# Optimization experiments

Measured on AMD Instinct MI355X. Metric: run time of the kernel, lower is better.

The kernel has to match this reference:

```python
import jax, jax.numpy as jnp
import numpy as np

B, N, D, H, T = 2048, 128, 256, 8, 64
HD = D // H
TANH_C = 10.0
MASK_PENALTY = 1e9


def setup_inputs() -> dict:
    key = jax.random.key(0)
    ks = jax.random.split(key, 16)
    s = 1.0 / np.sqrt(D).astype(np.float32)
    w = lambda k: jax.random.normal(k, (D, D), jnp.float32) * s
    return {
        'node_emb': jax.random.normal(ks[0], (B, N, D), jnp.float32),
        'graph_emb': jax.random.normal(ks[1], (B, D), jnp.float32),
        'W_target': w(ks[2]), 'W_global': w(ks[3]),
        'W_K1': w(ks[4]), 'W_K2': w(ks[5]),
        'W_Q': w(ks[6]), 'W_V': w(ks[7]),
        'Wq_m': w(ks[8]), 'Wk_m': w(ks[9]), 'Wv_m': w(ks[10]), 'Wo_m': w(ks[11]),
        'targets': jax.random.randint(ks[12], (T, B), 0, N, jnp.int32),
        'masks': jax.random.randint(ks[13], (T, B, N), 0, 2, jnp.int32),
    }


def _mha(q, k, v, Wq, Wk, Wv, Wo):
    # q: [B,1,D]; k,v: [B,N,D]. Standard multi-head attention (glimpse).
    qh = (q @ Wq.T).reshape(B, 1, H, HD).transpose(0, 2, 1, 3)   # [B,H,1,HD]
    kh = (k @ Wk.T).reshape(B, N, H, HD).transpose(0, 2, 1, 3)   # [B,H,N,HD]
    vh = (v @ Wv.T).reshape(B, N, H, HD).transpose(0, 2, 1, 3)
    scores = jnp.einsum('bhqd,bhnd->bhqn', qh, kh) / np.sqrt(HD).astype(np.float32)
    attn = jax.nn.softmax(scores, axis=-1)
    out = jnp.einsum('bhqn,bhnd->bhqd', attn, vh)                # [B,H,1,HD]
    out = out.transpose(0, 2, 1, 3).reshape(B, 1, D)
    return out @ Wo.T


def reference(node_emb, graph_emb, W_target, W_global, W_K1, W_K2, W_Q, W_V,
              Wq_m, Wk_m, Wv_m, Wo_m, targets, masks):
    # Step-invariant projections (embeddings fixed across decode steps here).
    keys = node_emb @ W_K1.T      # [B,N,D]
    vals = node_emb @ W_V.T       # [B,N,D]
    key2 = node_emb @ W_K2.T      # [B,N,D]
    g_ctx = graph_emb @ W_global.T  # [B,D]
    inv_sqrt_d = np.float32(1.0 / np.sqrt(D))

    def step(ll, tm):
        tgt, mask = tm  # tgt:[B] int32, mask:[B,N] int32
        tgt_emb = jnp.take_along_axis(node_emb, tgt[:, None, None], axis=1)[:, 0, :]  # [B,D]
        context = (tgt_emb @ W_target.T + g_ctx)[:, None, :]      # [B,1,D]
        glimpse = _mha(context, keys, vals, Wq_m, Wk_m, Wv_m, Wo_m)  # [B,1,D]
        query = glimpse @ W_Q.T                                    # [B,1,D]
        logits = jnp.einsum('bqd,bnd->bn', query, key2) * inv_sqrt_d  # [B,N]
        logits = TANH_C * jnp.tanh(logits) - mask.astype(jnp.float32) * MASK_PENALTY
        log_p = jax.nn.log_softmax(logits, axis=1)
        actions = jnp.argmax(log_p, axis=1)                        # greedy TopKSampler
        ll = ll + jnp.take_along_axis(log_p, actions[:, None], axis=1)[:, 0]
        return ll, None

    ll, _ = jax.lax.scan(step, jnp.zeros(B, jnp.float32), (targets, masks))
    return ll
```

## Files before the change

kernel.cpp:

```cpp
#include <hip/hip_runtime.h>
#include <hip/hip_bf16.h>

#define BB 2048
#define NN 128
#define DD 256
#define HH 8
#define TT 64

typedef __bf16 bf16x8 __attribute__((ext_vector_type(8)));
typedef float f32x4 __attribute__((ext_vector_type(4)));

static __device__ __forceinline__ f32x4 mfma16(bf16x8 a, bf16x8 b, f32x4 c) {
  return __builtin_amdgcn_mfma_f32_16x16x32_bf16(a, b, c, 0, 0, 0);
}

static __device__ __forceinline__ f32x4 zero4() {
  f32x4 z = {0.f, 0.f, 0.f, 0.f};
  return z;
}

static __device__ __forceinline__ bf16x8 cvt8(const float* p) {
  const float4 x0 = *(const float4*)p;
  const float4 x1 = *(const float4*)(p + 4);
  bf16x8 r;
  r[0] = (__bf16)x0.x; r[1] = (__bf16)x0.y; r[2] = (__bf16)x0.z; r[3] = (__bf16)x0.w;
  r[4] = (__bf16)x1.x; r[5] = (__bf16)x1.y; r[6] = (__bf16)x1.z; r[7] = (__bf16)x1.w;
  return r;
}

static __device__ __forceinline__ unsigned pk2(float a, float b) {
  __bf16 x = (__bf16)a, y = (__bf16)b;
  unsigned short ux, uy;
  __builtin_memcpy(&ux, &x, 2);
  __builtin_memcpy(&uy, &y, 2);
  return (unsigned)ux | ((unsigned)uy << 16);
}

static __device__ __forceinline__ float fast_tanh10(float y) {
  const float e = __expf(2.f * y);
  return 10.f - 20.f * __builtin_amdgcn_rcpf(1.f + e);
}

__global__ void fold1(const float* __restrict__ Wq_m, const float* __restrict__ W_target,
                      const float* __restrict__ W_global, const float* __restrict__ Wk_m,
                      const float* __restrict__ W_K1, const float* __restrict__ Wv_m,
                      const float* __restrict__ W_V, const float* __restrict__ W_Q,
                      const float* __restrict__ Wo_m,
                      __bf16* __restrict__ WTQ, float* __restrict__ WGQT,
                      __bf16* __restrict__ WKH, __bf16* __restrict__ WVH,
                      float* __restrict__ WQO) {
  const int p = blockIdx.x >> 8;
  const int i = blockIdx.x & 255;
  const int t = threadIdx.x;
  __shared__ float arow[256];
  const float* A;
  const float* Bm;
  if (p == 0)      { A = Wq_m; Bm = W_target; }
  else if (p == 1) { A = Wq_m; Bm = W_global; }
  else if (p == 2) { A = Wk_m; Bm = W_K1; }
  else if (p == 3) { A = Wv_m; Bm = W_V; }
  else             { A = W_Q;  Bm = Wo_m; }
  arow[t] = A[i * 256 + t];
  __syncthreads();
  float acc = 0.f;
  for (int k = 0; k < 256; ++k) acc = fmaf(arow[k], Bm[k * 256 + t], acc);
  if (p == 0)      WTQ[i * 256 + t] = (__bf16)acc;
  else if (p == 1) WGQT[t * 256 + i] = acc;
  else if (p == 2) WKH[i * 256 + t] = (__bf16)acc;
  else if (p == 3) WVH[i * 256 + t] = (__bf16)acc;
  else             WQO[i * 256 + t] = acc;
}

__global__ void fold2(const float* __restrict__ WQO, const float* __restrict__ W_K2,
                      __bf16* __restrict__ WZL) {
  const int j = blockIdx.x;
  const int t = threadIdx.x;
  __shared__ float col[256];
  col[t] = W_K2[t * 256 + j];
  __syncthreads();
  float acc = 0.f;
  for (int d = 0; d < 256; ++d) acc = fmaf(WQO[d * 256 + t], col[d], acc);
  WZL[j * 256 + t] = (__bf16)acc;
}

__global__ void gq_kernel(const float* __restrict__ ge, const float* __restrict__ WGQT,
                          float* __restrict__ GQ) {
  const int b0 = blockIdx.x * 8;
  const int t = threadIdx.x;
  __shared__ float g[8][256];
#pragma unroll
  for (int i = 0; i < 8; ++i) g[i][t] = ge[(b0 + i) * 256 + t];
  __syncthreads();
  float acc[8] = {0.f, 0.f, 0.f, 0.f, 0.f, 0.f, 0.f, 0.f};
  for (int j = 0; j < 256; ++j) {
    const float wv = WGQT[j * 256 + t];
#pragma unroll
    for (int i = 0; i < 8; ++i) acc[i] = fmaf(wv, g[i][j], acc[i]);
  }
#pragma unroll
  for (int i = 0; i < 8; ++i) GQ[(b0 + i) * 256 + t] = acc[i];
}

__global__ __launch_bounds__(256)
void kv_kernel(const float* __restrict__ E, const __bf16* __restrict__ WKH,
               const __bf16* __restrict__ WVH, __bf16* __restrict__ KH,
               __bf16* __restrict__ VT, __bf16* __restrict__ Ebf) {
  const int b = blockIdx.x;
  const int tid = threadIdx.x;
  const int w = tid >> 6;
  const int l = tid & 63;
  const int lr = l & 15;
  const int lg = l >> 4;
  __shared__ __align__(16) __bf16 Es[128 * 264];
  const float* Eb = E + (size_t)b * NN * DD;
  __bf16* Ebfb = Ebf + (size_t)b * NN * DD;
  for (int c = tid; c < 4096; c += 256) {
    const int row = c >> 5;
    const int c8 = c & 31;
    const bf16x8 v = cvt8(Eb + row * 256 + c8 * 8);
    *(bf16x8*)&Es[row * 264 + c8 * 8] = v;
    *(bf16x8*)(Ebfb + row * 256 + c8 * 8) = v;
  }
  __syncthreads();

  {
    f32x4 acc[8][4];
#pragma unroll
    for (int mf = 0; mf < 8; ++mf)
#pragma unroll
      for (int nf = 0; nf < 4; ++nf) acc[mf][nf] = zero4();
    for (int kk = 0; kk < 8; ++kk) {
      bf16x8 aF[8], bF[4];
#pragma unroll
      for (int mf = 0; mf < 8; ++mf)
        aF[mf] = *(const bf16x8*)&Es[(mf * 16 + lr) * 264 + kk * 32 + lg * 8];
#pragma unroll
      for (int nf = 0; nf < 4; ++nf)
        bF[nf] = *(const bf16x8*)(WKH + (size_t)(w * 64 + nf * 16 + lr) * DD + kk * 32 + lg * 8);
#pragma unroll
      for (int mf = 0; mf < 8; ++mf)
#pragma unroll
        for (int nf = 0; nf < 4; ++nf) acc[mf][nf] = mfma16(aF[mf], bF[nf], acc[mf][nf]);
    }
    __bf16* KHb = KH + (size_t)b * NN * DD;
#pragma unroll
    for (int mf = 0; mf < 8; ++mf)
#pragma unroll
      for (int nf = 0; nf < 4; ++nf)
#pragma unroll
        for (int r = 0; r < 4; ++r)
          KHb[(mf * 16 + lg * 4 + r) * DD + w * 64 + nf * 16 + lr] = (__bf16)acc[mf][nf][r];
  }

  {
    f32x4 acc[4][8];
#pragma unroll
    for (int mf = 0; mf < 4; ++mf)
#pragma unroll
      for (int nf = 0; nf < 8; ++nf) acc[mf][nf] = zero4();
    for (int kk = 0; kk < 8; ++kk) {
      bf16x8 aW[4], bE[8];
#pragma unroll
      for (int mf = 0; mf < 4; ++mf)
        aW[mf] = *(const bf16x8*)(WVH + (size_t)(w * 64 + mf * 16 + lr) * DD + kk * 32 + lg * 8);
#pragma unroll
      for (int nf = 0; nf < 8; ++nf)
        bE[nf] = *(const bf16x8*)&Es[(nf * 16 + lr) * 264 + kk * 32 + lg * 8];
#pragma unroll
      for (int mf = 0; mf < 4; ++mf)
#pragma unroll
        for (int nf = 0; nf < 8; ++nf) acc[mf][nf] = mfma16(aW[mf], bE[nf], acc[mf][nf]);
    }
    __bf16* VTb = VT + (size_t)b * DD * NN;
#pragma unroll
    for (int mf = 0; mf < 4; ++mf)
#pragma unroll
      for (int nf = 0; nf < 8; ++nf)
#pragma unroll
        for (int r = 0; r < 4; ++r)
          VTb[(w * 64 + mf * 16 + lg * 4 + r) * NN + nf * 16 + lr] = (__bf16)acc[mf][nf][r];
  }
}

__global__ __launch_bounds__(256)
void qproj_kernel(const __bf16* __restrict__ Ebf, const int* __restrict__ tg,
                  const __bf16* __restrict__ WTQ, const float* __restrict__ GQ,
                  __bf16* __restrict__ Qb) {
  const int b = blockIdx.x;
  const int tid = threadIdx.x;
  const int w = tid >> 6;
  const int l = tid & 63;
  const int lr = l & 15;
  const int lg = l >> 4;
  __shared__ __align__(16) __bf16 Qst[64 * 264];
  __shared__ int tgs[64];
  if (tid < 64) tgs[tid] = tg[tid * BB + b];
  __syncthreads();
  const __bf16* Eb = Ebf + (size_t)b * NN * DD;
#pragma unroll
  for (int it = 0; it < 8; ++it) {
    const int c = it * 256 + tid;
    const int row = c >> 5;
    const int c8 = c & 31;
    *(bf16x8*)&Qst[row * 264 + c8 * 8] =
        *(const bf16x8*)(Eb + (size_t)tgs[row] * DD + c8 * 8);
  }
  __syncthreads();

  f32x4 acc[4][4];
#pragma unroll
  for (int mf = 0; mf < 4; ++mf)
#pragma unroll
    for (int nf = 0; nf < 4; ++nf) acc[mf][nf] = zero4();
  for (int kk = 0; kk < 8; ++kk) {
    bf16x8 aF[4], bF[4];
#pragma unroll
    for (int mf = 0; mf < 4; ++mf)
      aF[mf] = *(const bf16x8*)&Qst[(mf * 16 + lr) * 264 + kk * 32 + lg * 8];
#pragma unroll
    for (int nf = 0; nf < 4; ++nf)
      bF[nf] = *(const bf16x8*)(WTQ + (size_t)(w * 64 + nf * 16 + lr) * DD + kk * 32 + lg * 8);
#pragma unroll
    for (int mf = 0; mf < 4; ++mf)
#pragma unroll
      for (int nf = 0; nf < 4; ++nf) acc[mf][nf] = mfma16(aF[mf], bF[nf], acc[mf][nf]);
  }
#pragma unroll
  for (int nf = 0; nf < 4; ++nf) {
    const int col = w * 64 + nf * 16 + lr;
    const float g = GQ[b * DD + col];
#pragma unroll
    for (int mf = 0; mf < 4; ++mf)
#pragma unroll
      for (int r = 0; r < 4; ++r)
        Qb[((size_t)b * TT + mf * 16 + lg * 4 + r) * DD + col] = (__bf16)(acc[mf][nf][r] + g);
  }
}

__global__ __launch_bounds__(256)
void attn4_kernel(const __bf16* __restrict__ Qb, const __bf16* __restrict__ KH,
                  const __bf16* __restrict__ VT, __bf16* __restrict__ HO) {
  const int b = blockIdx.x >> 2;
  const int c0 = (blockIdx.x & 3) * 64;
  const int tid = threadIdx.x;
  const int w = tid >> 6;
  const int l = tid & 63;
  const int lr = l & 15;
  const int lg = l >> 4;
  const int T0 = w * 16;

  __shared__ __align__(16) __bf16 KHs[128 * 72];
  __shared__ __align__(16) __bf16 VTs[64 * 136];
  __shared__ __align__(16) __bf16 Ps[4][16 * 136];

  const __bf16* KHb = KH + (size_t)b * NN * DD;
  const __bf16* VTb = VT + (size_t)b * DD * NN;

#pragma unroll
  for (int it = 0; it < 4; ++it) {
    const int c = it * 256 + tid;
    const int row = c >> 3;
    const int c8 = c & 7;
    *(bf16x8*)&KHs[row * 72 + c8 * 8] = *(const bf16x8*)(KHb + (size_t)row * DD + c0 + c8 * 8);
  }
#pragma unroll
  for (int it = 0; it < 4; ++it) {
    const int c = it * 256 + tid;
    const int row = c >> 4;
    const int c8 = c & 15;
    *(bf16x8*)&VTs[row * 136 + c8 * 8] =
        *(const bf16x8*)(VTb + (size_t)(c0 + row) * NN + c8 * 8);
  }
  __syncthreads();

  __bf16* myp = Ps[w];
  __bf16* HOb = HO + (size_t)b * TT * DD + c0;

#pragma unroll
  for (int h = 0; h < 2; ++h) {
    const bf16x8 aq =
        *(const bf16x8*)(Qb + ((size_t)b * TT + T0 + lr) * DD + c0 + h * 32 + lg * 8);
    f32x4 s[8];
#pragma unroll
    for (int nf = 0; nf < 8; ++nf)
      s[nf] = mfma16(*(const bf16x8*)&KHs[(nf * 16 + lr) * 72 + h * 32 + lg * 8], aq, zero4());

    float mx = -1e30f;
#pragma unroll
    for (int nf = 0; nf < 8; ++nf)
#pragma unroll
      for (int r = 0; r < 4; ++r) mx = fmaxf(mx, s[nf][r]);
    mx = fmaxf(mx, __shfl_xor(mx, 16));
    mx = fmaxf(mx, __shfl_xor(mx, 32));

    float sm = 0.f;
    uint2 evp[8];
#pragma unroll
    for (int nf = 0; nf < 8; ++nf) {
      const float e0 = __expf((s[nf][0] - mx) * 0.17677669529663687f);
      const float e1 = __expf((s[nf][1] - mx) * 0.17677669529663687f);
      const float e2 = __expf((s[nf][2] - mx) * 0.17677669529663687f);
      const float e3 = __expf((s[nf][3] - mx) * 0.17677669529663687f);
      sm += (e0 + e1) + (e2 + e3);
      evp[nf].x = pk2(e0, e1);
      evp[nf].y = pk2(e2, e3);
    }
    sm += __shfl_xor(sm, 16);
    sm += __shfl_xor(sm, 32);

#pragma unroll
    for (int nf = 0; nf < 8; ++nf)
      *(uint2*)&myp[lr * 136 + nf * 16 + lg * 4] = evp[nf];

    f32x4 o0 = zero4(), o1 = zero4();
#pragma unroll
    for (int kk = 0; kk < 4; ++kk) {
      const bf16x8 ap = *(const bf16x8*)&myp[lr * 136 + kk * 32 + lg * 8];
      o0 = mfma16(ap, *(const bf16x8*)&VTs[(h * 32 + lr) * 136 + kk * 32 + lg * 8], o0);
      o1 = mfma16(ap, *(const bf16x8*)&VTs[(h * 32 + 16 + lr) * 136 + kk * 32 + lg * 8], o1);
    }
#pragma unroll
    for (int r = 0; r < 4; ++r) {
      const float inv = __builtin_amdgcn_rcpf(__shfl(sm, lg * 4 + r));
      HOb[(size_t)(T0 + lg * 4 + r) * DD + h * 32 + lr] = (__bf16)(o0[r] * inv);
      HOb[(size_t)(T0 + lg * 4 + r) * DD + h * 32 + 16 + lr] = (__bf16)(o1[r] * inv);
    }
  }
}

__global__ __launch_bounds__(256)
void zlog2_kernel(const __bf16* __restrict__ Ebf, const __bf16* __restrict__ HO,
                  const __bf16* __restrict__ WZL, const int* __restrict__ MK,
                  float* __restrict__ out) {
  const int b = blockIdx.x;
  const int tid = threadIdx.x;
  const int w = tid >> 6;
  const int l = tid & 63;
  const int lr = l & 15;
  const int lg = l >> 4;
  const int T0 = w * 16;
  __shared__ __align__(16) __bf16 Zs[64 * 264];
  __shared__ float red[4];

  const __bf16* Eb = Ebf + (size_t)b * NN * DD;
  const __bf16* HOb = HO + (size_t)b * TT * DD;

  {
    f32x4 acc[4][4];
#pragma unroll
    for (int mf = 0; mf < 4; ++mf)
#pragma unroll
      for (int nf = 0; nf < 4; ++nf) acc[mf][nf] = zero4();
    for (int kk = 0; kk < 8; ++kk) {
      bf16x8 aF[4], bF[4];
#pragma unroll
      for (int mf = 0; mf < 4; ++mf)
        aF[mf] = *(const bf16x8*)(HOb + (size_t)(mf * 16 + lr) * DD + kk * 32 + lg * 8);
#pragma unroll
      for (int nf = 0; nf < 4; ++nf)
        bF[nf] = *(const bf16x8*)(WZL + (size_t)(w * 64 + nf * 16 + lr) * DD + kk * 32 + lg * 8);
#pragma unroll
      for (int mf = 0; mf < 4; ++mf)
#pragma unroll
        for (int nf = 0; nf < 4; ++nf) acc[mf][nf] = mfma16(aF[mf], bF[nf], acc[mf][nf]);
    }
#pragma unroll
    for (int mf = 0; mf < 4; ++mf)
#pragma unroll
      for (int nf = 0; nf < 4; ++nf)
#pragma unroll
        for (int r = 0; r < 4; ++r)
          Zs[(mf * 16 + lg * 4 + r) * 264 + w * 64 + nf * 16 + lr] = (__bf16)acc[mf][nf][r];
  }
  __syncthreads();

  {
    f32x4 sa[8];
#pragma unroll
    for (int nf = 0; nf < 8; ++nf) sa[nf] = zero4();
    for (int kk = 0; kk < 8; ++kk) {
      const bf16x8 bZ = *(const bf16x8*)&Zs[(T0 + lr) * 264 + kk * 32 + lg * 8];
#pragma unroll
      for (int nf = 0; nf < 8; ++nf) {
        const bf16x8 aE = *(const bf16x8*)(Eb + (size_t)(nf * 16 + lr) * DD + kk * 32 + lg * 8);
        sa[nf] = mfma16(aE, bZ, sa[nf]);
      }
    }
    const int t = T0 + lr;
    float xs[8][4];
    float mx = -3e38f;
#pragma unroll
    for (int nf = 0; nf < 8; ++nf) {
      const int4 mk4 = *(const int4*)(MK + ((size_t)t * BB + b) * NN + nf * 16 + lg * 4);
      xs[nf][0] = fast_tanh10(sa[nf][0] * 0.0625f) - (float)mk4.x * 1e9f;
      xs[nf][1] = fast_tanh10(sa[nf][1] * 0.0625f) - (float)mk4.y * 1e9f;
      xs[nf][2] = fast_tanh10(sa[nf][2] * 0.0625f) - (float)mk4.z * 1e9f;
      xs[nf][3] = fast_tanh10(sa[nf][3] * 0.0625f) - (float)mk4.w * 1e9f;
      mx = fmaxf(mx, fmaxf(fmaxf(xs[nf][0], xs[nf][1]), fmaxf(xs[nf][2], xs[nf][3])));
    }
    mx = fmaxf(mx, __shfl_xor(mx, 16));
    mx = fmaxf(mx, __shfl_xor(mx, 32));
    float sm = 0.f;
#pragma unroll
    for (int nf = 0; nf < 8; ++nf)
#pragma unroll
      for (int r = 0; r < 4; ++r) sm += __expf(xs[nf][r] - mx);
    sm += __shfl_xor(sm, 16);
    sm += __shfl_xor(sm, 32);
    float part = logf(sm);
    part += __shfl_xor(part, 1);
    part += __shfl_xor(part, 2);
    part += __shfl_xor(part, 4);
    part += __shfl_xor(part, 8);
    if (l == 0) red[w] = part;
  }
  __syncthreads();
  if (tid == 0) out[b] = -(red[0] + red[1] + red[2] + red[3]);
}

extern "C" void kernel_launch(void* const* d_in, const int* in_sizes, int n_in,
                              void* d_out, int out_size, void* d_ws, size_t ws_size,
                              hipStream_t stream) {
  (void)in_sizes; (void)n_in; (void)out_size; (void)ws_size;
  const float* node_emb  = (const float*)d_in[0];
  const float* graph_emb = (const float*)d_in[1];
  const float* W_target  = (const float*)d_in[2];
  const float* W_global  = (const float*)d_in[3];
  const float* W_K1      = (const float*)d_in[4];
  const float* W_K2      = (const float*)d_in[5];
  const float* W_Q       = (const float*)d_in[6];
  const float* W_V       = (const float*)d_in[7];
  const float* Wq_m      = (const float*)d_in[8];
  const float* Wk_m      = (const float*)d_in[9];
  const float* Wv_m      = (const float*)d_in[10];
  const float* Wo_m      = (const float*)d_in[11];
  const int* targets     = (const int*)d_in[12];
  const int* masks       = (const int*)d_in[13];

  char* p = (char*)d_ws;
  __bf16* Ebf = (__bf16*)p; p += (size_t)BB * NN * DD * 2;
  __bf16* KH  = (__bf16*)p; p += (size_t)BB * NN * DD * 2;
  __bf16* VT  = (__bf16*)p; p += (size_t)BB * DD * NN * 2;
  __bf16* HO  = (__bf16*)p; p += (size_t)BB * TT * DD * 2;
  __bf16* Qb  = (__bf16*)p; p += (size_t)BB * TT * DD * 2;
  __bf16* WTQ = (__bf16*)p; p += 256 * 256 * 2;
  __bf16* WKH = (__bf16*)p; p += 256 * 256 * 2;
  __bf16* WVH = (__bf16*)p; p += 256 * 256 * 2;
  __bf16* WZL = (__bf16*)p; p += 256 * 256 * 2;
  float* WGQT = (float*)p;  p += 256 * 256 * 4;
  float* WQO  = (float*)p;  p += 256 * 256 * 4;
  float* GQ   = (float*)p;  p += (size_t)BB * DD * 4;

  fold1<<<1280, 256, 0, stream>>>(Wq_m, W_target, W_global, Wk_m, W_K1, Wv_m, W_V, W_Q, Wo_m,
                                  WTQ, WGQT, WKH, WVH, WQO);
  fold2<<<256, 256, 0, stream>>>(WQO, W_K2, WZL);
  gq_kernel<<<BB / 8, 256, 0, stream>>>(graph_emb, WGQT, GQ);
  kv_kernel<<<BB, 256, 0, stream>>>(node_emb, WKH, WVH, KH, VT, Ebf);
  qproj_kernel<<<BB, 256, 0, stream>>>(Ebf, targets, WTQ, GQ, Qb);
  attn4_kernel<<<BB * 4, 256, 0, stream>>>(Qb, KH, VT, HO);
  zlog2_kernel<<<BB, 256, 0, stream>>>(Ebf, HO, WZL, masks, (float*)d_out);
}
```

Baseline: 571.4 us.

## Fuse target-query projection into K/V projection kernel with 512-thread blocks

Merges qproj_kernel into the K/V projection kernel so the gathered target rows come straight from the bf16 node tile already in shared memory. This avoids a kernel launch and the global re-read of Ebf for the 64 gathered rows. The block grows from 256 to 512 threads, so each wave covers 32 output columns instead of 64. The larger block lowers per-wave register pressure but may change occupancy, and the target loads into shared memory now rely on the existing barrier after the tile fill.

```diff
diff --git a/kernel.cpp b/kernel.cpp
--- a/kernel.cpp
+++ b/kernel.cpp
@@ -101,10 +101,12 @@
   for (int i = 0; i < 8; ++i) GQ[(b0 + i) * 256 + t] = acc[i];
 }
 
-__global__ __launch_bounds__(256)
-void kv_kernel(const float* __restrict__ E, const __bf16* __restrict__ WKH,
-               const __bf16* __restrict__ WVH, __bf16* __restrict__ KH,
-               __bf16* __restrict__ VT, __bf16* __restrict__ Ebf) {
+__global__ __launch_bounds__(512)
+void kvq_kernel(const float* __restrict__ E, const int* __restrict__ tg,
+                const __bf16* __restrict__ WKH, const __bf16* __restrict__ WVH,
+                const __bf16* __restrict__ WTQ, const float* __restrict__ GQ,
+                __bf16* __restrict__ KH, __bf16* __restrict__ VT,
+                __bf16* __restrict__ Qb, __bf16* __restrict__ Ebf) {
   const int b = blockIdx.x;
   const int tid = threadIdx.x;
   const int w = tid >> 6;
@@ -112,9 +114,13 @@
   const int lr = l & 15;
   const int lg = l >> 4;
   __shared__ __align__(16) __bf16 Es[128 * 264];
+  __shared__ int tgs[64];
+  if (tid < 64) tgs[tid] = tg[tid * BB + b];
   const float* Eb = E + (size_t)b * NN * DD;
   __bf16* Ebfb = Ebf + (size_t)b * NN * DD;
-  for (int c = tid; c < 4096; c += 256) {
+#pragma unroll
+  for (int it = 0; it < 8; ++it) {
+    const int c = it * 512 + tid;
     const int row = c >> 5;
     const int c8 = c & 31;
     const bf16x8 v = cvt8(Eb + row * 256 + c8 * 8);
@@ -124,116 +130,95 @@
   __syncthreads();
 
   {
-    f32x4 acc[8][4];
+    f32x4 acc[8][2];
 #pragma unroll
     for (int mf = 0; mf < 8; ++mf)
 #pragma unroll
-      for (int nf = 0; nf < 4; ++nf) acc[mf][nf] = zero4();
+      for (int nf = 0; nf < 2; ++nf) acc[mf][nf] = zero4();
     for (int kk = 0; kk < 8; ++kk) {
-      bf16x8 aF[8], bF[4];
+      bf16x8 aF[8], bF[2];
 #pragma unroll
       for (int mf = 0; mf < 8; ++mf)
         aF[mf] = *(const bf16x8*)&Es[(mf * 16 + lr) * 264 + kk * 32 + lg * 8];
 #pragma unroll
-      for (int nf = 0; nf < 4; ++nf)
-        bF[nf] = *(const bf16x8*)(WKH + (size_t)(w * 64 + nf * 16 + lr) * DD + kk * 32 + lg * 8);
+      for (int nf = 0; nf < 2; ++nf)
+        bF[nf] = *(const bf16x8*)(WKH + (size_t)(w * 32 + nf * 16 + lr) * DD + kk * 32 + lg * 8);
 #pragma unroll
       for (int mf = 0; mf < 8; ++mf)
 #pragma unroll
-        for (int nf = 0; nf < 4; ++nf) acc[mf][nf] = mfma16(aF[mf], bF[nf], acc[mf][nf]);
+        for (int nf = 0; nf < 2; ++nf) acc[mf][nf] = mfma16(aF[mf], bF[nf], acc[mf][nf]);
     }
     __bf16* KHb = KH + (size_t)b * NN * DD;
 #pragma unroll
     for (int mf = 0; mf < 8; ++mf)
 #pragma unroll
-      for (int nf = 0; nf < 4; ++nf)
+      for (int nf = 0; nf < 2; ++nf)
 #pragma unroll
         for (int r = 0; r < 4; ++r)
-          KHb[(mf * 16 + lg * 4 + r) * DD + w * 64 + nf * 16 + lr] = (__bf16)acc[mf][nf][r];
+          KHb[(mf * 16 + lg * 4 + r) * DD + w * 32 + nf * 16 + lr] = (__bf16)acc[mf][nf][r];
   }
 
   {
-    f32x4 acc[4][8];
-#pragma unroll
-    for (int mf = 0; mf < 4; ++mf)
+    f32x4 acc[2][8];
+#pragma unroll
+    for (int mf = 0; mf < 2; ++mf)
 #pragma unroll
       for (int nf = 0; nf < 8; ++nf) acc[mf][nf] = zero4();
     for (int kk = 0; kk < 8; ++kk) {
-      bf16x8 aW[4], bE[8];
-#pragma unroll
-      for (int mf = 0; mf < 4; ++mf)
-        aW[mf] = *(const bf16x8*)(WVH + (size_t)(w * 64 + mf * 16 + lr) * DD + kk * 32 + lg * 8);
+      bf16x8 aW[2], bE[8];
+#pragma unroll
+      for (int mf = 0; mf < 2; ++mf)
+        aW[mf] = *(const bf16x8*)(WVH + (size_t)(w * 32 + mf * 16 + lr) * DD + kk * 32 + lg * 8);
 #pragma unroll
       for (int nf = 0; nf < 8; ++nf)
         bE[nf] = *(const bf16x8*)&Es[(nf * 16 + lr) * 264 + kk * 32 + lg * 8];
 #pragma unroll
+      for (int mf = 0; mf < 2; ++mf)
+#pragma unroll
+        for (int nf = 0; nf < 8; ++nf) acc[mf][nf] = mfma16(aW[mf], bE[nf], acc[mf][nf]);
+    }
+    __bf16* VTb = VT + (size_t)b * DD * NN;
+#pragma unroll
+    for (int mf = 0; mf < 2; ++mf)
+#pragma unroll
+      for (int nf = 0; nf < 8; ++nf)
+#pragma unroll
+        for (int r = 0; r < 4; ++r)
+          VTb[(w * 32 + mf * 16 + lg * 4 + r) * NN + nf * 16 + lr] = (__bf16)acc[mf][nf][r];
+  }
+
+  {
+    f32x4 acc[4][2];
+#pragma unroll
+    for (int mf = 0; mf < 4; ++mf)
+#pragma unroll
+      for (int nf = 0; nf < 2; ++nf) acc[mf][nf] = zero4();
+    int rowoff[4];
+#pragma unroll
+    for (int mf = 0; mf < 4; ++mf) rowoff[mf] = tgs[mf * 16 + lr] * 264;
+    for (int kk = 0; kk < 8; ++kk) {
+      bf16x8 aF[4], bF[2];
+#pragma unroll
       for (int mf = 0; mf < 4; ++mf)
-#pragma unroll
-        for (int nf = 0; nf < 8; ++nf) acc[mf][nf] = mfma16(aW[mf], bE[nf], acc[mf][nf]);
-    }
-    __bf16* VTb = VT + (size_t)b * DD * NN;
-#pragma unroll
-    for (int mf = 0; mf < 4; ++mf)
-#pragma unroll
-      for (int nf = 0; nf < 8; ++nf)
+        aF[mf] = *(const bf16x8*)&Es[rowoff[mf] + kk * 32 + lg * 8];
+#pragma unroll
+      for (int nf = 0; nf < 2; ++nf)
+        bF[nf] = *(const bf16x8*)(WTQ + (size_t)(w * 32 + nf * 16 + lr) * DD + kk * 32 + lg * 8);
+#pragma unroll
+      for (int mf = 0; mf < 4; ++mf)
+#pragma unroll
+        for (int nf = 0; nf < 2; ++nf) acc[mf][nf] = mfma16(aF[mf], bF[nf], acc[mf][nf]);
+    }
+#pragma unroll
+    for (int nf = 0; nf < 2; ++nf) {
+      const int col = w * 32 + nf * 16 + lr;
+      const float g = GQ[b * DD + col];
+#pragma unroll
+      for (int mf = 0; mf < 4; ++mf)
 #pragma unroll
         for (int r = 0; r < 4; ++r)
-          VTb[(w * 64 + mf * 16 + lg * 4 + r) * NN + nf * 16 + lr] = (__bf16)acc[mf][nf][r];
-  }
-}
-
-__global__ __launch_bounds__(256)
-void qproj_kernel(const __bf16* __restrict__ Ebf, const int* __restrict__ tg,
-                  const __bf16* __restrict__ WTQ, const float* __restrict__ GQ,
-                  __bf16* __restrict__ Qb) {
-  const int b = blockIdx.x;
-  const int tid = threadIdx.x;
-  const int w = tid >> 6;
-  const int l = tid & 63;
-  const int lr = l & 15;
-  const int lg = l >> 4;
-  __shared__ __align__(16) __bf16 Qst[64 * 264];
-  __shared__ int tgs[64];
-  if (tid < 64) tgs[tid] = tg[tid * BB + b];
-  __syncthreads();
-  const __bf16* Eb = Ebf + (size_t)b * NN * DD;
-#pragma unroll
-  for (int it = 0; it < 8; ++it) {
-    const int c = it * 256 + tid;
-    const int row = c >> 5;
-    const int c8 = c & 31;
-    *(bf16x8*)&Qst[row * 264 + c8 * 8] =
-        *(const bf16x8*)(Eb + (size_t)tgs[row] * DD + c8 * 8);
-  }
-  __syncthreads();
-
-  f32x4 acc[4][4];
-#pragma unroll
-  for (int mf = 0; mf < 4; ++mf)
-#pragma unroll
-    for (int nf = 0; nf < 4; ++nf) acc[mf][nf] = zero4();
-  for (int kk = 0; kk < 8; ++kk) {
-    bf16x8 aF[4], bF[4];
-#pragma unroll
-    for (int mf = 0; mf < 4; ++mf)
-      aF[mf] = *(const bf16x8*)&Qst[(mf * 16 + lr) * 264 + kk * 32 + lg * 8];
-#pragma unroll
-    for (int nf = 0; nf < 4; ++nf)
-      bF[nf] = *(const bf16x8*)(WTQ + (size_t)(w * 64 + nf * 16 + lr) * DD + kk * 32 + lg * 8);
-#pragma unroll
-    for (int mf = 0; mf < 4; ++mf)
-#pragma unroll
-      for (int nf = 0; nf < 4; ++nf) acc[mf][nf] = mfma16(aF[mf], bF[nf], acc[mf][nf]);
-  }
-#pragma unroll
-  for (int nf = 0; nf < 4; ++nf) {
-    const int col = w * 64 + nf * 16 + lr;
-    const float g = GQ[b * DD + col];
-#pragma unroll
-    for (int mf = 0; mf < 4; ++mf)
-#pragma unroll
-      for (int r = 0; r < 4; ++r)
-        Qb[((size_t)b * TT + mf * 16 + lg * 4 + r) * DD + col] = (__bf16)(acc[mf][nf][r] + g);
+          Qb[((size_t)b * TT + mf * 16 + lg * 4 + r) * DD + col] = (__bf16)(acc[mf][nf][r] + g);
+    }
   }
 }
 
@@ -455,8 +440,7 @@
                                   WTQ, WGQT, WKH, WVH, WQO);
   fold2<<<256, 256, 0, stream>>>(WQO, W_K2, WZL);
   gq_kernel<<<BB / 8, 256, 0, stream>>>(graph_emb, WGQT, GQ);
-  kv_kernel<<<BB, 256, 0, stream>>>(node_emb, WKH, WVH, KH, VT, Ebf);
-  qproj_kernel<<<BB, 256, 0, stream>>>(Ebf, targets, WTQ, GQ, Qb);
+  kvq_kernel<<<BB, 512, 0, stream>>>(node_emb, targets, WKH, WVH, WTQ, GQ, KH, VT, Qb, Ebf);
   attn4_kernel<<<BB * 4, 256, 0, stream>>>(Qb, KH, VT, HO);
   zlog2_kernel<<<BB, 256, 0, stream>>>(Ebf, HO, WZL, masks, (float*)d_out);
 }
```

Measured after the change: 513.2 us. -10.2%, faster.
